# Optimization experiments

Measured on AMD Instinct MI355X. Metric: run time of the kernel, lower is better.

Reference implementation:

```python
import jax, jax.numpy as jnp
import numpy as np

N = 100000   # nodes
D = 128      # in_feats
H = 128      # hidden_size
E = 500000   # message edges
EP = 100000  # positive pair edges
EN = 500000  # negative pair edges


def setup_inputs() -> dict:
    key = jax.random.key(0)
    ks = jax.random.split(key, 20)
    s = 1.0 / np.sqrt(H)
    f32 = jnp.float32
    inp = {
        "x": jax.random.normal(ks[0], (N, D), f32),
        "src": jax.random.randint(ks[1], (E,), 0, N, jnp.int32),
        "dst": jax.random.randint(ks[2], (E,), 0, N, jnp.int32),
        "pos_src": jax.random.randint(ks[3], (EP,), 0, N, jnp.int32),
        "pos_dst": jax.random.randint(ks[4], (EP,), 0, N, jnp.int32),
        "neg_src": jax.random.randint(ks[5], (EN,), 0, N, jnp.int32),
        "neg_dst": jax.random.randint(ks[6], (EN,), 0, N, jnp.int32),
        # SAGEConv layer 0 (in->hid) and layer 1 (hid->hid)
        "W_self0": jax.random.normal(ks[7], (D, H), f32) * s,
        "W_neigh0": jax.random.normal(ks[8], (D, H), f32) * s,
        "b0": jnp.zeros((H,), f32),
        "W_self1": jax.random.normal(ks[9], (H, H), f32) * s,
        "W_neigh1": jax.random.normal(ks[10], (H, H), f32) * s,
        "b1": jnp.zeros((H,), f32),
        # EdgeDecoder MLP: hid->hid->hid->1
        "dW1": jax.random.normal(ks[11], (H, H), f32) * s,
        "db1": jnp.zeros((H,), f32),
        "dW2": jax.random.normal(ks[12], (H, H), f32) * s,
        "db2": jnp.zeros((H,), f32),
        "dW3": jax.random.normal(ks[13], (H, 1), f32) * s,
        "db3": jnp.zeros((1,), f32),
    }
    return inp


def _sage_mean(h, src, dst, W_self, W_neigh, b, n_nodes):
    # mean-aggregate neighbor features: gather src feats, segment-sum over dst
    agg = jax.ops.segment_sum(h[src], dst, num_segments=n_nodes)       # [N, d]
    deg = jax.ops.segment_sum(jnp.ones((src.shape[0],), h.dtype), dst,
                              num_segments=n_nodes)                     # [N]
    h_neigh = agg / jnp.maximum(deg, 1.0)[:, None]
    return h @ W_self + h_neigh @ W_neigh + b


def _edge_decode(h, e_src, e_dst, W1, b1, W2, b2, W3, b3):
    z = h[e_src] * h[e_dst]                    # [E_pair, H]
    z = jax.nn.relu(z @ W1 + b1)
    z = jax.nn.relu(z @ W2 + b2)
    return z @ W3 + b3                         # [E_pair, 1]


def reference(x, src, dst, pos_src, pos_dst, neg_src, neg_dst,
              W_self0, W_neigh0, b0, W_self1, W_neigh1, b1,
              dW1, db1, dW2, db2, dW3, db3):
    n = x.shape[0]
    h = jax.nn.relu(_sage_mean(x, src, dst, W_self0, W_neigh0, b0, n))
    h = _sage_mean(h, src, dst, W_self1, W_neigh1, b1, n)  # no act on last layer
    h_pos = _edge_decode(h, pos_src, pos_dst, dW1, db1, dW2, db2, dW3, db3)
    h_neg = _edge_decode(h, neg_src, neg_dst, dW1, db1, dW2, db2, dW3, db3)
    return (h_pos, h_neg)
```

## Files before the change

### kernel.cpp

```cpp
#include <hip/hip_runtime.h>
#include <hip/hip_bf16.h>

#define HD 128

typedef unsigned int u32;
typedef unsigned short u16;
typedef __attribute__((ext_vector_type(8))) short short8;
typedef __attribute__((ext_vector_type(4))) float f32x4;

__device__ __forceinline__ float bf2f(u16 u) {
    return __uint_as_float(((u32)u) << 16);
}
__device__ __forceinline__ u16 f2bf(float f) {
    u32 u = __float_as_uint(f);
    u32 r = (u + 0x7fffu + ((u >> 16) & 1u)) >> 16;
    return (u16)r;
}
__device__ __forceinline__ u32 pk2bf(float lo, float hi) {
    __hip_bfloat162 h = __float22bfloat162_rn(make_float2(lo, hi));
    union { __hip_bfloat162 h; u32 u; } cv; cv.h = h;
    return cv.u;
}
__device__ __forceinline__ u32 hmul2(u32 a, u32 b) {
    union { u32 u; __hip_bfloat162 h; } x, y, r;
    x.u = a; y.u = b;
    r.h = __hmul2(x.h, y.h);
    return r.u;
}
__device__ __forceinline__ float ldf(const void* p, size_t i, bool f32m) {
    return f32m ? ((const float*)p)[i] : bf2f(((const u16*)p)[i]);
}
__device__ __forceinline__ int swz(int row, int col) {
    return row * 128 + ((((col >> 3) ^ (row & 7)) << 3) | (col & 7));
}

__global__ void detect_mode(const u32* __restrict__ x, int* __restrict__ mode) {
    __shared__ int cnt_s;
    if (threadIdx.x == 0) cnt_s = 0;
    __syncthreads();
    u32 e = (x[threadIdx.x] >> 23) & 0xFFu;
    if (e >= 90u && e < 170u) atomicAdd(&cnt_s, 1);
    __syncthreads();
    if (threadIdx.x == 0) mode[0] = (cnt_s >= 128) ? 1 : 0;
}

__global__ void pack_w6(const void* __restrict__ W0, const void* __restrict__ W1,
                        const void* __restrict__ W2, const void* __restrict__ W3,
                        const void* __restrict__ W4, const void* __restrict__ W5,
                        u16* __restrict__ out, const int* __restrict__ gmode) {
    const bool f32m = gmode[0] != 0;
    int gid = blockIdx.x * 256 + threadIdx.x;
    if (gid >= 6 * 16384) return;
    int sel = gid >> 14, idx = gid & 16383;
    const void* W = sel == 0 ? W0 : sel == 1 ? W1 : sel == 2 ? W2 :
                    sel == 3 ? W3 : sel == 4 ? W4 : W5;
    int j = idx & 7, lane = (idx >> 3) & 63, ks = (idx >> 9) & 3, nt = idx >> 11;
    int k = ks * 32 + (lane >> 4) * 8 + j;
    int n = nt * 16 + (lane & 15);
    out[gid] = f2bf(ldf(W, (size_t)k * HD + n, f32m));
}

__global__ void cnt_count(const int* __restrict__ dst, int* __restrict__ cnt, int e) {
    int i = blockIdx.x * 256 + threadIdx.x;
    if (i < e) atomicAdd(&cnt[dst[i]], 1);
}

__global__ void scan_blocks(const int* __restrict__ cnt, int* __restrict__ rowptr,
                            int* __restrict__ bsum, int n) {
    __shared__ int s[256];
    int t = threadIdx.x, gid = blockIdx.x * 256 + t;
    int v = (gid < n) ? cnt[gid] : 0;
    s[t] = v; __syncthreads();
    #pragma unroll
    for (int off = 1; off < 256; off <<= 1) {
        int x = (t >= off) ? s[t - off] : 0;
        __syncthreads();
        s[t] += x;
        __syncthreads();
    }
    if (gid < n) rowptr[gid] = s[t] - v;
    if (t == 255) bsum[blockIdx.x] = s[255];
}

__global__ void scan_bsum(int* __restrict__ bsum, int nb) {
    __shared__ int s[1024];
    __shared__ int carry;
    int t = threadIdx.x;
    if (t == 0) carry = 0;
    __syncthreads();
    for (int base = 0; base < nb; base += 1024) {
        int i = base + t;
        int v = (i < nb) ? bsum[i] : 0;
        s[t] = v; __syncthreads();
        #pragma unroll
        for (int off = 1; off < 1024; off <<= 1) {
            int x = (t >= off) ? s[t - off] : 0;
            __syncthreads();
            s[t] += x;
            __syncthreads();
        }
        if (i < nb) bsum[i] = carry + s[t] - v;
        __syncthreads();
        if (t == 0) carry += s[1023];
        __syncthreads();
    }
}

__global__ void scan_add(int* __restrict__ rowptr, const int* __restrict__ bsum,
                         int* __restrict__ cur, int n, int e) {
    int gid = blockIdx.x * 256 + threadIdx.x;
    if (gid < n) {
        int v = rowptr[gid] + bsum[blockIdx.x];
        rowptr[gid] = v;
        cur[gid] = v;
    } else if (gid == n) {
        rowptr[n] = e;
    }
}

__global__ void csr_fill(const int* __restrict__ src, const int* __restrict__ dst,
                         int* __restrict__ cur, int* __restrict__ cidx, int e) {
    int i = blockIdx.x * 256 + threadIdx.x;
    if (i >= e) return;
    int p = atomicAdd(&cur[dst[i]], 1);
    cidx[p] = src[i];
}

__global__ __launch_bounds__(256) void agg_gather(
    const void* __restrict__ h, const int* __restrict__ rowptr,
    const int* __restrict__ cidx, u16* __restrict__ aggb,
    const int* __restrict__ gmode, int use_mode, int n) {
    const bool f32m = use_mode && (gmode[0] != 0);
    int wid = (blockIdx.x * 256 + threadIdx.x) >> 6;
    int lane = threadIdx.x & 63;
    if (wid >= n) return;
    int l16 = lane & 15, g = lane >> 4;
    int s0 = rowptr[wid], s1 = rowptr[wid + 1];
    float acc[8] = {0.f, 0.f, 0.f, 0.f, 0.f, 0.f, 0.f, 0.f};
    for (int i = s0 + g; i < s1; i += 4) {
        int s = cidx[i];
        if (f32m) {
            const float* p = (const float*)h + (size_t)s * HD + l16 * 8;
            float4 a = *(const float4*)p, b = *(const float4*)(p + 4);
            acc[0] += a.x; acc[1] += a.y; acc[2] += a.z; acc[3] += a.w;
            acc[4] += b.x; acc[5] += b.y; acc[6] += b.z; acc[7] += b.w;
        } else {
            uint4 v = *(const uint4*)((const u16*)h + (size_t)s * HD + l16 * 8);
            acc[0] += __uint_as_float(v.x << 16); acc[1] += __uint_as_float(v.x & 0xffff0000u);
            acc[2] += __uint_as_float(v.y << 16); acc[3] += __uint_as_float(v.y & 0xffff0000u);
            acc[4] += __uint_as_float(v.z << 16); acc[5] += __uint_as_float(v.z & 0xffff0000u);
            acc[6] += __uint_as_float(v.w << 16); acc[7] += __uint_as_float(v.w & 0xffff0000u);
        }
    }
    #pragma unroll
    for (int k = 0; k < 8; k++) {
        acc[k] += __shfl_xor(acc[k], 16);
        acc[k] += __shfl_xor(acc[k], 32);
    }
    if (g == 0) {
        float iv = 1.f / fmaxf((float)(s1 - s0), 1.f);
        uint4 o;
        o.x = pk2bf(acc[0] * iv, acc[1] * iv);
        o.y = pk2bf(acc[2] * iv, acc[3] * iv);
        o.z = pk2bf(acc[4] * iv, acc[5] * iv);
        o.w = pk2bf(acc[6] * iv, acc[7] * iv);
        *(uint4*)&aggb[(size_t)wid * HD + l16 * 8] = o;
    }
}

template <bool RELU>
__global__ __launch_bounds__(256) void sage_mfma(
    const void* __restrict__ X, const u16* __restrict__ aggb,
    const u16* __restrict__ Wsp, const u16* __restrict__ Wnp,
    const void* __restrict__ bias, u16* __restrict__ hout,
    const int* __restrict__ gmode, int use_mode, int n) {
    __shared__ u16 z[64 * 128];
    const bool f32m = gmode[0] != 0;
    const bool inf32 = use_mode && f32m;
    const int t = threadIdx.x;
    const int n0 = blockIdx.x * 64;
    const int lane = t & 63;
    const int w = t >> 6;
    const int cl = lane & 15, quad = lane >> 4;

    #pragma unroll
    for (int i = 0; i < 4; i++) {
        int idx = t + i * 256;
        int e = idx >> 4, sg = (idx & 15) * 8;
        int node = n0 + e;
        uint4 p = make_uint4(0, 0, 0, 0);
        if (node < n) {
            if (inf32) {
                const float* xp = (const float*)X + (size_t)node * HD + sg;
                float4 v0 = *(const float4*)xp, v1 = *(const float4*)(xp + 4);
                p.x = pk2bf(v0.x, v0.y); p.y = pk2bf(v0.z, v0.w);
                p.z = pk2bf(v1.x, v1.y); p.w = pk2bf(v1.z, v1.w);
            } else {
                p = *(const uint4*)((const u16*)X + (size_t)node * HD + sg);
            }
        }
        *(uint4*)&z[swz(e, sg)] = p;
    }
    __syncthreads();

    f32x4 acc[2][4];
    #pragma unroll
    for (int ft = 0; ft < 2; ft++) {
        int f0 = w * 32 + ft * 16 + quad * 4;
        f32x4 bv;
        bv[0] = ldf(bias, f0 + 0, f32m);
        bv[1] = ldf(bias, f0 + 1, f32m);
        bv[2] = ldf(bias, f0 + 2, f32m);
        bv[3] = ldf(bias, f0 + 3, f32m);
        #pragma unroll
        for (int et = 0; et < 4; et++) acc[ft][et] = bv;
    }
    #pragma unroll
    for (int ks = 0; ks < 4; ks++) {
        short8 a[2], b[4];
        #pragma unroll
        for (int ft = 0; ft < 2; ft++)
            a[ft] = ((const short8*)Wsp)[((w * 2 + ft) * 4 + ks) * 64 + lane];
        #pragma unroll
        for (int et = 0; et < 4; et++)
            b[et] = *(const short8*)&z[swz(et * 16 + cl, ks * 32 + quad * 8)];
        #pragma unroll
        for (int ft = 0; ft < 2; ft++)
            #pragma unroll
            for (int et = 0; et < 4; et++)
                acc[ft][et] = __builtin_amdgcn_mfma_f32_16x16x32_bf16(
                    a[ft], b[et], acc[ft][et], 0, 0, 0);
    }
    __syncthreads();

    #pragma unroll
    for (int i = 0; i < 4; i++) {
        int idx = t + i * 256;
        int e = idx >> 4, sg = (idx & 15) * 8;
        int node = n0 + e;
        uint4 q = make_uint4(0, 0, 0, 0);
        if (node < n) q = *(const uint4*)&aggb[(size_t)node * HD + sg];
        *(uint4*)&z[swz(e, sg)] = q;
    }
    __syncthreads();
    #pragma unroll
    for (int ks = 0; ks < 4; ks++) {
        short8 a[2], b[4];
        #pragma unroll
        for (int ft = 0; ft < 2; ft++)
            a[ft] = ((const short8*)Wnp)[((w * 2 + ft) * 4 + ks) * 64 + lane];
        #pragma unroll
        for (int et = 0; et < 4; et++)
            b[et] = *(const short8*)&z[swz(et * 16 + cl, ks * 32 + quad * 8)];
        #pragma unroll
        for (int ft = 0; ft < 2; ft++)
            #pragma unroll
            for (int et = 0; et < 4; et++)
                acc[ft][et] = __builtin_amdgcn_mfma_f32_16x16x32_bf16(
                    a[ft], b[et], acc[ft][et], 0, 0, 0);
    }
    __syncthreads();

    #pragma unroll
    for (int ft = 0; ft < 2; ft++) {
        int f0 = w * 32 + ft * 16 + quad * 4;
        #pragma unroll
        for (int et = 0; et < 4; et++) {
            f32x4 v = acc[ft][et];
            float v0 = RELU ? fmaxf(v[0], 0.f) : v[0];
            float v1 = RELU ? fmaxf(v[1], 0.f) : v[1];
            float v2 = RELU ? fmaxf(v[2], 0.f) : v[2];
            float v3 = RELU ? fmaxf(v[3], 0.f) : v[3];
            *(uint2*)&z[swz(et * 16 + cl, f0)] =
                make_uint2(pk2bf(v0, v1), pk2bf(v2, v3));
        }
    }
    __syncthreads();
    #pragma unroll
    for (int i = 0; i < 4; i++) {
        int idx = t + i * 256;
        int e = idx >> 4, sg = (idx & 15) * 8;
        int node = n0 + e;
        if (node < n)
            *(uint4*)&hout[(size_t)node * HD + sg] = *(const uint4*)&z[swz(e, sg)];
    }
}

__global__ __launch_bounds__(256) void edge_decode_mfma(
    const u16* __restrict__ h,
    const int* __restrict__ psrc, const int* __restrict__ pdst, int ep, int PB,
    const int* __restrict__ nsrc, const int* __restrict__ ndst, int en,
    const u16* __restrict__ W1p, const void* __restrict__ b1,
    const u16* __restrict__ W2p, const void* __restrict__ b2,
    const void* __restrict__ W3, const void* __restrict__ b3,
    void* __restrict__ out, const int* __restrict__ gmode) {
    __shared__ u16 zA[64 * 128];
    __shared__ float psum[256];
    const bool f32m = gmode[0] != 0;
    const int t = threadIdx.x;
    const int b = blockIdx.x;
    const int* esrc; const int* edst; int e0, obase, ne;
    if (b < PB) { esrc = psrc; edst = pdst; e0 = b * 64;        obase = 0;  ne = ep; }
    else        { esrc = nsrc; edst = ndst; e0 = (b - PB) * 64; obase = ep; ne = en; }
    const int lane = t & 63;
    const int w = t >> 6;
    const int cl = lane & 15, quad = lane >> 4;

    #pragma unroll
    for (int i = 0; i < 4; i++) {
        int idx = t + i * 256;
        int e = idx >> 4, sg = (idx & 15) * 8;
        int eg = e0 + e;
        uint4 z = make_uint4(0, 0, 0, 0);
        if (eg < ne) {
            int s = esrc[eg], d = edst[eg];
            uint4 a  = *(const uint4*)(h + (size_t)s * HD + sg);
            uint4 bv = *(const uint4*)(h + (size_t)d * HD + sg);
            z.x = hmul2(a.x, bv.x); z.y = hmul2(a.y, bv.y);
            z.z = hmul2(a.z, bv.z); z.w = hmul2(a.w, bv.w);
        }
        *(uint4*)&zA[swz(e, sg)] = z;
    }
    __syncthreads();

    f32x4 acc[2][4];
    #pragma unroll
    for (int ft = 0; ft < 2; ft++) {
        int f0 = w * 32 + ft * 16 + quad * 4;
        f32x4 bv;
        bv[0] = ldf(b1, f0 + 0, f32m);
        bv[1] = ldf(b1, f0 + 1, f32m);
        bv[2] = ldf(b1, f0 + 2, f32m);
        bv[3] = ldf(b1, f0 + 3, f32m);
        #pragma unroll
        for (int et = 0; et < 4; et++) acc[ft][et] = bv;
    }
    #pragma unroll
    for (int ks = 0; ks < 4; ks++) {
        short8 a[2], bb[4];
        #pragma unroll
        for (int ft = 0; ft < 2; ft++)
            a[ft] = ((const short8*)W1p)[((w * 2 + ft) * 4 + ks) * 64 + lane];
        #pragma unroll
        for (int et = 0; et < 4; et++)
            bb[et] = *(const short8*)&zA[swz(et * 16 + cl, ks * 32 + quad * 8)];
        #pragma unroll
        for (int ft = 0; ft < 2; ft++)
            #pragma unroll
            for (int et = 0; et < 4; et++)
                acc[ft][et] = __builtin_amdgcn_mfma_f32_16x16x32_bf16(
                    a[ft], bb[et], acc[ft][et], 0, 0, 0);
    }
    __syncthreads();

    #pragma unroll
    for (int ft = 0; ft < 2; ft++) {
        int f0 = w * 32 + ft * 16 + quad * 4;
        #pragma unroll
        for (int et = 0; et < 4; et++) {
            f32x4 v = acc[ft][et];
            *(uint2*)&zA[swz(et * 16 + cl, f0)] = make_uint2(
                pk2bf(fmaxf(v[0], 0.f), fmaxf(v[1], 0.f)),
                pk2bf(fmaxf(v[2], 0.f), fmaxf(v[3], 0.f)));
        }
    }
    __syncthreads();

    #pragma unroll
    for (int ft = 0; ft < 2; ft++) {
        int f0 = w * 32 + ft * 16 + quad * 4;
        f32x4 bv;
        bv[0] = ldf(b2, f0 + 0, f32m);
        bv[1] = ldf(b2, f0 + 1, f32m);
        bv[2] = ldf(b2, f0 + 2, f32m);
        bv[3] = ldf(b2, f0 + 3, f32m);
        #pragma unroll
        for (int et = 0; et < 4; et++) acc[ft][et] = bv;
    }
    #pragma unroll
    for (int ks = 0; ks < 4; ks++) {
        short8 a[2], bb[4];
        #pragma unroll
        for (int ft = 0; ft < 2; ft++)
            a[ft] = ((const short8*)W2p)[((w * 2 + ft) * 4 + ks) * 64 + lane];
        #pragma unroll
        for (int et = 0; et < 4; et++)
            bb[et] = *(const short8*)&zA[swz(et * 16 + cl, ks * 32 + quad * 8)];
        #pragma unroll
        for (int ft = 0; ft < 2; ft++)
            #pragma unroll
            for (int et = 0; et < 4; et++)
                acc[ft][et] = __builtin_amdgcn_mfma_f32_16x16x32_bf16(
                    a[ft], bb[et], acc[ft][et], 0, 0, 0);
    }
    float p[4] = {0.f, 0.f, 0.f, 0.f};
    #pragma unroll
    for (int ft = 0; ft < 2; ft++) {
        int f0 = w * 32 + ft * 16 + quad * 4;
        float w3v0 = ldf(W3, f0 + 0, f32m);
        float w3v1 = ldf(W3, f0 + 1, f32m);
        float w3v2 = ldf(W3, f0 + 2, f32m);
        float w3v3 = ldf(W3, f0 + 3, f32m);
        #pragma unroll
        for (int et = 0; et < 4; et++) {
            f32x4 v = acc[ft][et];
            p[et] = fmaf(fmaxf(v[0], 0.f), w3v0, p[et]);
            p[et] = fmaf(fmaxf(v[1], 0.f), w3v1, p[et]);
            p[et] = fmaf(fmaxf(v[2], 0.f), w3v2, p[et]);
            p[et] = fmaf(fmaxf(v[3], 0.f), w3v3, p[et]);
        }
    }
    #pragma unroll
    for (int et = 0; et < 4; et++) {
        p[et] += __shfl_xor(p[et], 16);
        p[et] += __shfl_xor(p[et], 32);
    }
    if (lane < 16) {
        #pragma unroll
        for (int et = 0; et < 4; et++)
            psum[w * 64 + et * 16 + lane] = p[et];
    }
    __syncthreads();
    if (t < 64) {
        int eg = e0 + t;
        if (eg < ne) {
            float sum = ldf(b3, 0, f32m) + (psum[t] + psum[64 + t])
                      + (psum[128 + t] + psum[192 + t]);
            if (f32m) ((float*)out)[obase + eg] = sum;
            else      ((u16*)out)[obase + eg]   = f2bf(sum);
        }
    }
}

extern "C" void kernel_launch(void* const* d_in, const int* in_sizes, int n_in,
                              void* d_out, int out_size, void* d_ws, size_t ws_size,
                              hipStream_t stream) {
    const void* x      = d_in[0];
    const int* src     = (const int*)d_in[1];
    const int* dst     = (const int*)d_in[2];
    const int* pos_src = (const int*)d_in[3];
    const int* pos_dst = (const int*)d_in[4];
    const int* neg_src = (const int*)d_in[5];
    const int* neg_dst = (const int*)d_in[6];
    const void* Ws0 = d_in[7];
    const void* Wn0 = d_in[8];
    const void* b0  = d_in[9];
    const void* Ws1 = d_in[10];
    const void* Wn1 = d_in[11];
    const void* b1  = d_in[12];
    const void* dW1 = d_in[13];
    const void* db1 = d_in[14];
    const void* dW2 = d_in[15];
    const void* db2 = d_in[16];
    const void* dW3 = d_in[17];
    const void* db3 = d_in[18];

    const int n  = in_sizes[0] / HD;
    const int e  = in_sizes[1];
    const int ep = in_sizes[3];
    const int en = in_sizes[5];
    const int NB = (n + 255) / 256;
    const int PB = (ep + 63) / 64, NDB = (en + 63) / 64;

    char* base = (char*)d_ws;
    u16* aggb = (u16*)d_ws;
    u16* h1   = aggb + (size_t)n * HD;
    size_t off = (size_t)n * HD * 4;
    int* mode = (int*)(base + off);      off += 16;
    int* rowptr = (int*)(base + off);    off += (size_t)(n + 1) * 4; off = (off + 15) & ~(size_t)15;
    int* cur = (int*)(base + off);       off += (size_t)n * 4;       off = (off + 15) & ~(size_t)15;
    int* cidx = (int*)(base + off);      off += (size_t)e * 4;       off = (off + 15) & ~(size_t)15;
    int* bsum = (int*)(base + off);      off += (size_t)NB * 4;      off = (off + 15) & ~(size_t)15;
    u16* Wpk  = (u16*)(base + off);
    u16* W1p  = Wpk;
    u16* W2p  = Wpk + 16384;
    u16* Ws0p = Wpk + 2 * 16384;
    u16* Wn0p = Wpk + 3 * 16384;
    u16* Ws1p = Wpk + 4 * 16384;
    u16* Wn1p = Wpk + 5 * 16384;

    detect_mode<<<dim3(1), dim3(256), 0, stream>>>((const u32*)x, mode);

    hipMemsetAsync(cur, 0, (size_t)n * 4, stream);
    cnt_count<<<dim3((e + 255) / 256), dim3(256), 0, stream>>>(dst, cur, e);
    scan_blocks<<<dim3(NB), dim3(256), 0, stream>>>(cur, rowptr, bsum, n);
    scan_bsum<<<dim3(1), dim3(1024), 0, stream>>>(bsum, NB);
    scan_add<<<dim3((n + 256) / 256), dim3(256), 0, stream>>>(rowptr, bsum, cur, n, e);
    csr_fill<<<dim3((e + 255) / 256), dim3(256), 0, stream>>>(src, dst, cur, cidx, e);

    pack_w6<<<dim3(384), dim3(256), 0, stream>>>(dW1, dW2, Ws0, Wn0, Ws1, Wn1, Wpk, mode);

    agg_gather<<<dim3((n * 64 + 255) / 256), dim3(256), 0, stream>>>(
        x, rowptr, cidx, aggb, mode, 1, n);
    sage_mfma<true><<<dim3((n + 63) / 64), dim3(256), 0, stream>>>(
        x, aggb, Ws0p, Wn0p, b0, h1, mode, 1, n);

    agg_gather<<<dim3((n * 64 + 255) / 256), dim3(256), 0, stream>>>(
        h1, rowptr, cidx, aggb, mode, 0, n);
    sage_mfma<false><<<dim3((n + 63) / 64), dim3(256), 0, stream>>>(
        h1, aggb, Ws1p, Wn1p, b1, aggb , mode, 0, n);

    edge_decode_mfma<<<dim3(PB + NDB), dim3(256), 0, stream>>>(
        aggb, pos_src, pos_dst, ep, PB, neg_src, neg_dst, en,
        W1p, db1, W2p, db2, dW3, db3, d_out, mode);
}
```

Before: 364.9 us.

## Fuse neighbor mean aggregation into SAGE MFMA kernel, drop agg buffer

Removes the separate agg_gather kernel and computes each node's neighbor mean directly inside sage_mfma, writing it straight into shared memory before the neighbor GEMM. This avoids writing and re-reading an N×128 bf16 aggregate buffer and saves two kernel launches. In exchange, each 16-lane group walks a whole node's edge list sequentially, unrolled by two, which gives less memory-level parallelism per wave than the old layout of four edges in flight per node and can leave the MFMA blocks stalled on gather latency.

```diff
diff --git a/kernel.cpp b/kernel.cpp
--- a/kernel.cpp
+++ b/kernel.cpp
@@ -32,6 +32,12 @@
 }
 __device__ __forceinline__ int swz(int row, int col) {
     return row * 128 + ((((col >> 3) ^ (row & 7)) << 3) | (col & 7));
+}
+__device__ __forceinline__ void acc8_bf16(uint4 v, float* a) {
+    a[0] += __uint_as_float(v.x << 16); a[1] += __uint_as_float(v.x & 0xffff0000u);
+    a[2] += __uint_as_float(v.y << 16); a[3] += __uint_as_float(v.y & 0xffff0000u);
+    a[4] += __uint_as_float(v.z << 16); a[5] += __uint_as_float(v.z & 0xffff0000u);
+    a[6] += __uint_as_float(v.w << 16); a[7] += __uint_as_float(v.w & 0xffff0000u);
 }
 
 __global__ void detect_mode(const u32* __restrict__ x, int* __restrict__ mode) {
@@ -126,51 +132,10 @@
     cidx[p] = src[i];
 }
 
-__global__ __launch_bounds__(256) void agg_gather(
-    const void* __restrict__ h, const int* __restrict__ rowptr,
-    const int* __restrict__ cidx, u16* __restrict__ aggb,
-    const int* __restrict__ gmode, int use_mode, int n) {
-    const bool f32m = use_mode && (gmode[0] != 0);
-    int wid = (blockIdx.x * 256 + threadIdx.x) >> 6;
-    int lane = threadIdx.x & 63;
-    if (wid >= n) return;
-    int l16 = lane & 15, g = lane >> 4;
-    int s0 = rowptr[wid], s1 = rowptr[wid + 1];
-    float acc[8] = {0.f, 0.f, 0.f, 0.f, 0.f, 0.f, 0.f, 0.f};
-    for (int i = s0 + g; i < s1; i += 4) {
-        int s = cidx[i];
-        if (f32m) {
-            const float* p = (const float*)h + (size_t)s * HD + l16 * 8;
-            float4 a = *(const float4*)p, b = *(const float4*)(p + 4);
-            acc[0] += a.x; acc[1] += a.y; acc[2] += a.z; acc[3] += a.w;
-            acc[4] += b.x; acc[5] += b.y; acc[6] += b.z; acc[7] += b.w;
-        } else {
-            uint4 v = *(const uint4*)((const u16*)h + (size_t)s * HD + l16 * 8);
-            acc[0] += __uint_as_float(v.x << 16); acc[1] += __uint_as_float(v.x & 0xffff0000u);
-            acc[2] += __uint_as_float(v.y << 16); acc[3] += __uint_as_float(v.y & 0xffff0000u);
-            acc[4] += __uint_as_float(v.z << 16); acc[5] += __uint_as_float(v.z & 0xffff0000u);
-            acc[6] += __uint_as_float(v.w << 16); acc[7] += __uint_as_float(v.w & 0xffff0000u);
-        }
-    }
-    #pragma unroll
-    for (int k = 0; k < 8; k++) {
-        acc[k] += __shfl_xor(acc[k], 16);
-        acc[k] += __shfl_xor(acc[k], 32);
-    }
-    if (g == 0) {
-        float iv = 1.f / fmaxf((float)(s1 - s0), 1.f);
-        uint4 o;
-        o.x = pk2bf(acc[0] * iv, acc[1] * iv);
-        o.y = pk2bf(acc[2] * iv, acc[3] * iv);
-        o.z = pk2bf(acc[4] * iv, acc[5] * iv);
-        o.w = pk2bf(acc[6] * iv, acc[7] * iv);
-        *(uint4*)&aggb[(size_t)wid * HD + l16 * 8] = o;
-    }
-}
-
 template <bool RELU>
 __global__ __launch_bounds__(256) void sage_mfma(
-    const void* __restrict__ X, const u16* __restrict__ aggb,
+    const void* __restrict__ X, const int* __restrict__ rowptr,
+    const int* __restrict__ cidx,
     const u16* __restrict__ Wsp, const u16* __restrict__ Wnp,
     const void* __restrict__ bias, u16* __restrict__ hout,
     const int* __restrict__ gmode, int use_mode, int n) {
@@ -182,6 +147,7 @@
     const int lane = t & 63;
     const int w = t >> 6;
     const int cl = lane & 15, quad = lane >> 4;
+    const int l16 = lane & 15, g = lane >> 4;
 
     #pragma unroll
     for (int i = 0; i < 4; i++) {
@@ -233,16 +199,56 @@
     }
     __syncthreads();
 
-    #pragma unroll
-    for (int i = 0; i < 4; i++) {
-        int idx = t + i * 256;
-        int e = idx >> 4, sg = (idx & 15) * 8;
+    #pragma unroll 1
+    for (int r = 0; r < 4; r++) {
+        int e = w * 16 + r * 4 + g;
         int node = n0 + e;
-        uint4 q = make_uint4(0, 0, 0, 0);
-        if (node < n) q = *(const uint4*)&aggb[(size_t)node * HD + sg];
-        *(uint4*)&z[swz(e, sg)] = q;
-    }
-    __syncthreads();
+        float a[8] = {0.f, 0.f, 0.f, 0.f, 0.f, 0.f, 0.f, 0.f};
+        int deg = 0;
+        if (node < n) {
+            int s0 = rowptr[node], s1 = rowptr[node + 1];
+            deg = s1 - s0;
+            int i = s0;
+            if (inf32) {
+                for (; i + 1 < s1; i += 2) {
+                    const float* pA = (const float*)X + (size_t)cidx[i] * HD + l16 * 8;
+                    const float* pB = (const float*)X + (size_t)cidx[i + 1] * HD + l16 * 8;
+                    float4 a0 = *(const float4*)pA, a1 = *(const float4*)(pA + 4);
+                    float4 b0 = *(const float4*)pB, b1 = *(const float4*)(pB + 4);
+                    a[0] += a0.x + b0.x; a[1] += a0.y + b0.y;
+                    a[2] += a0.z + b0.z; a[3] += a0.w + b0.w;
+                    a[4] += a1.x + b1.x; a[5] += a1.y + b1.y;
+                    a[6] += a1.z + b1.z; a[7] += a1.w + b1.w;
+                }
+                if (i < s1) {
+                    const float* pA = (const float*)X + (size_t)cidx[i] * HD + l16 * 8;
+                    float4 a0 = *(const float4*)pA, a1 = *(const float4*)(pA + 4);
+                    a[0] += a0.x; a[1] += a0.y; a[2] += a0.z; a[3] += a0.w;
+                    a[4] += a1.x; a[5] += a1.y; a[6] += a1.z; a[7] += a1.w;
+                }
+            } else {
+                for (; i + 1 < s1; i += 2) {
+                    uint4 vA = *(const uint4*)((const u16*)X + (size_t)cidx[i] * HD + l16 * 8);
+                    uint4 vB = *(const uint4*)((const u16*)X + (size_t)cidx[i + 1] * HD + l16 * 8);
+                    acc8_bf16(vA, a);
+                    acc8_bf16(vB, a);
+                }
+                if (i < s1) {
+                    uint4 vA = *(const uint4*)((const u16*)X + (size_t)cidx[i] * HD + l16 * 8);
+                    acc8_bf16(vA, a);
+                }
+            }
+        }
+        float iv = 1.f / fmaxf((float)deg, 1.f);
+        uint4 o;
+        o.x = pk2bf(a[0] * iv, a[1] * iv);
+        o.y = pk2bf(a[2] * iv, a[3] * iv);
+        o.z = pk2bf(a[4] * iv, a[5] * iv);
+        o.w = pk2bf(a[6] * iv, a[7] * iv);
+        *(uint4*)&z[swz(e, l16 * 8)] = o;
+    }
+    __syncthreads();
+
     #pragma unroll
     for (int ks = 0; ks < 4; ks++) {
         short8 a[2], b[4];
@@ -463,8 +469,8 @@
     const int PB = (ep + 63) / 64, NDB = (en + 63) / 64;
 
     char* base = (char*)d_ws;
-    u16* aggb = (u16*)d_ws;
-    u16* h1   = aggb + (size_t)n * HD;
+    u16* h2 = (u16*)d_ws;
+    u16* h1 = h2 + (size_t)n * HD;
     size_t off = (size_t)n * HD * 4;
     int* mode = (int*)(base + off);      off += 16;
     int* rowptr = (int*)(base + off);    off += (size_t)(n + 1) * 4; off = (off + 15) & ~(size_t)15;
@@ -490,17 +496,13 @@
 
     pack_w6<<<dim3(384), dim3(256), 0, stream>>>(dW1, dW2, Ws0, Wn0, Ws1, Wn1, Wpk, mode);
 
-    agg_gather<<<dim3((n * 64 + 255) / 256), dim3(256), 0, stream>>>(
-        x, rowptr, cidx, aggb, mode, 1, n);
     sage_mfma<true><<<dim3((n + 63) / 64), dim3(256), 0, stream>>>(
-        x, aggb, Ws0p, Wn0p, b0, h1, mode, 1, n);
-
-    agg_gather<<<dim3((n * 64 + 255) / 256), dim3(256), 0, stream>>>(
-        h1, rowptr, cidx, aggb, mode, 0, n);
+        x, rowptr, cidx, Ws0p, Wn0p, b0, h1, mode, 1, n);
+
     sage_mfma<false><<<dim3((n + 63) / 64), dim3(256), 0, stream>>>(
-        h1, aggb, Ws1p, Wn1p, b1, aggb , mode, 0, n);
+        h1, rowptr, cidx, Ws1p, Wn1p, b1, h2, mode, 0, n);
 
     edge_decode_mfma<<<dim3(PB + NDB), dim3(256), 0, stream>>>(
-        aggb, pos_src, pos_dst, ep, PB, neg_src, neg_dst, en,
+        h2, pos_src, pos_dst, ep, PB, neg_src, neg_dst, en,
         W1p, db1, W2p, db2, dW3, db3, d_out, mode);
 }
```

Measured after the change: 346.7 us. 1.05x faster.
